# Optimization experiments

Hardware: AMD Instinct MI355X
Metric: run time of the kernel (lower is better)

## Reference

```python
import jax, jax.numpy as jnp
import numpy as np

N = 100000
E = 1600000
IN_F, HID, OUT_F = 256, 128, 64


def setup_inputs() -> dict:
    key = jax.random.key(0)
    k_x, k_e, k_w1, k_w2, k_b1, k_b2 = jax.random.split(key, 6)
    x = jax.random.normal(k_x, (N, IN_F), dtype=jnp.float32)
    edge_index = jax.random.randint(k_e, (2, E), 0, N, dtype=jnp.int32)
    # GCNConv params: lin has no bias in PyG; separate additive bias per layer.
    W1 = jax.random.normal(k_w1, (IN_F, HID), dtype=jnp.float32) / np.sqrt(IN_F)
    b1 = jax.random.normal(k_b1, (HID,), dtype=jnp.float32) * 0.01
    W2 = jax.random.normal(k_w2, (HID, OUT_F), dtype=jnp.float32) / np.sqrt(HID)
    b2 = jax.random.normal(k_b2, (OUT_F,), dtype=jnp.float32) * 0.01
    return {"x": x, "edge_index": edge_index, "W1": W1, "b1": b1, "W2": W2, "b2": b2}


def _gcn_norm(edge_index, num_nodes):
    # add self loops (improved=False -> weight 1.0), symmetric normalization
    loop = jnp.arange(num_nodes, dtype=edge_index.dtype)
    src = jnp.concatenate([edge_index[0], loop])
    dst = jnp.concatenate([edge_index[1], loop])
    w = jnp.ones(src.shape[0], dtype=jnp.float32)
    deg = jax.ops.segment_sum(w, dst, num_segments=num_nodes)
    dinv = jnp.where(deg > 0, jax.lax.rsqrt(deg), 0.0)
    norm = dinv[src] * w * dinv[dst]
    return src, dst, norm


def _gcn_layer(h, W, b, src, dst, norm, num_nodes):
    h = h @ W                               # [N, out]
    msg = h[src] * norm[:, None]            # [E+N, out] gather + scale
    out = jax.ops.segment_sum(msg, dst, num_segments=num_nodes)  # scatter-add
    return out + b


def reference(x, edge_index, W1, b1, W2, b2):
    # dropout is identity in eval mode
    src, dst, norm = _gcn_norm(edge_index, N)
    h = _gcn_layer(x, W1, b1, src, dst, norm, N)
    h = jax.nn.relu(h)
    out = _gcn_layer(h, W2, b2, src, dst, norm, N)
    return out
```

## Files before the change

### kernel.cpp

```cpp
#include <hip/hip_runtime.h>
#include <hip/hip_bf16.h>

#define N_NODES 100000
#define N_EDGES 1600000
#define IN_FEAT 256
#define HID_F   128
#define OUT_FT  64

#define NBUK   256
#define NPB    391
#define BUKCAP 8192
#define EPB    4096
#define G_BIN  ((N_EDGES + EPB - 1) / EPB)
#define G_GEMM ((N_NODES + 63) / 64)
#define G_CAST ((IN_FEAT * HID_F + HID_F * OUT_FT + 255) / 256)
#define G_AGG  ((N_NODES + 7) / 8)

typedef unsigned short u16;
typedef __attribute__((ext_vector_type(8))) unsigned short u16x8;
typedef __attribute__((ext_vector_type(8))) short short8;
typedef __attribute__((ext_vector_type(4))) float f32x4;

static __device__ inline u16 f2bf(float f) {
    __hip_bfloat16 h = __float2bfloat16(f);
    return *reinterpret_cast<u16*>(&h);
}
static __device__ inline float bf2f(u16 u) {
    union { unsigned u; float f; } c;
    c.u = ((unsigned)u) << 16;
    return c.f;
}


__global__ __launch_bounds__(256) void k_bin(const int* __restrict__ srcA,
                                             const int* __restrict__ dstA,
                                             int* __restrict__ gcur, unsigned* __restrict__ pairs,
                                             const float* __restrict__ W1,
                                             const float* __restrict__ W2,
                                             u16* __restrict__ W1t, u16* __restrict__ W2t) {
    if (blockIdx.x >= G_BIN) {
        int idx = (blockIdx.x - G_BIN) * 256 + threadIdx.x;
        if (idx < IN_FEAT * HID_F) {
            int k = idx / HID_F, n = idx % HID_F;
            W1t[n * IN_FEAT + k] = f2bf(W1[idx]);
        } else {
            int e2 = idx - IN_FEAT * HID_F;
            if (e2 < HID_F * OUT_FT) {
                int k = e2 / OUT_FT, n = e2 % OUT_FT;
                W2t[n * HID_F + k] = f2bf(W2[e2]);
            }
        }
        return;
    }
    __shared__ int lh[NBUK];
    int t = threadIdx.x;
    int e0 = blockIdx.x * EPB;
    if (t < NBUK) lh[t] = 0;
    __syncthreads();
#pragma unroll
    for (int i = 0; i < EPB / 256; i++) {
        int e = e0 + i * 256 + t;
        if (e < N_EDGES) atomicAdd(&lh[dstA[e] / NPB], 1);
    }
    __syncthreads();
    if (t < NBUK) {
        int c = lh[t];
        lh[t] = atomicAdd(&gcur[t], c);
    }
    __syncthreads();
#pragma unroll
    for (int i = 0; i < EPB / 256; i++) {
        int e = e0 + i * 256 + t;
        if (e < N_EDGES) {
            int d = dstA[e];
            int b = d / NPB;
            int p = atomicAdd(&lh[b], 1);
            if (p < BUKCAP) {
                unsigned packed = ((unsigned)(d - b * NPB) << 17) | (unsigned)srcA[e];
                pairs[(size_t)b * BUKCAP + p] = packed;
            }
        }
    }
}


__global__ __launch_bounds__(256) void k_fillB(const unsigned* __restrict__ pairs,
                                               const int* __restrict__ gcnt,
                                               int* __restrict__ offsets,
                                               float* __restrict__ dinv,
                                               int* __restrict__ csr) {
    __shared__ int hist[NPB];
    __shared__ int sm[256];
    __shared__ int s_ebase;
    int b = blockIdx.x, t = threadIdx.x;
    int nbase = b * NPB;
    int nn = min(NPB, N_NODES - nbase);

    int gv = gcnt[t];
    sm[t] = gv;
    __syncthreads();
    for (int o = 1; o < 256; o <<= 1) {
        int u = (t >= o) ? sm[t - o] : 0;
        __syncthreads();
        sm[t] += u;
        __syncthreads();
    }
    if (t == b) s_ebase = sm[t] - gv;
    __syncthreads();
    int ebase = s_ebase;
    int cnt = gcnt[b];
    const unsigned* pb = pairs + (size_t)b * BUKCAP;

    for (int i = t; i < NPB; i += 256) hist[i] = 0;
    __syncthreads();
    for (int i = t; i < cnt; i += 256) atomicAdd(&hist[pb[i] >> 17], 1);
    __syncthreads();

    int base2 = t * 2;
    int c0 = (base2 < NPB) ? hist[base2] : 0;
    int c1 = (base2 + 1 < NPB) ? hist[base2 + 1] : 0;
    int s = c0 + c1;
    __syncthreads();
    sm[t] = s;
    __syncthreads();
    for (int o = 1; o < 256; o <<= 1) {
        int u = (t >= o) ? sm[t - o] : 0;
        __syncthreads();
        sm[t] += u;
        __syncthreads();
    }
    int run = ebase + sm[t] - s;
    __syncthreads();
    int cc[2] = {c0, c1};
#pragma unroll
    for (int q = 0; q < 2; q++) {
        int n = base2 + q;
        if (n < nn) {
            int g = nbase + n;
            offsets[g] = run;
            dinv[g] = rsqrtf((float)(cc[q] + 1));
            hist[n] = run;
            run += cc[q];
        }
    }
    __syncthreads();
    for (int i = t; i < cnt; i += 256) {
        unsigned e = pb[i];
        int p = atomicAdd(&hist[e >> 17], 1);
        csr[p] = (int)(e & 0x1FFFFu);
    }
    if (b == NBUK - 1 && t == 0) offsets[N_NODES] = N_EDGES;
}


__global__ __launch_bounds__(256) void k_gemm1(const float* __restrict__ A,
                                               const u16* __restrict__ Bt,
                                               const float* __restrict__ dinv,
                                               u16* __restrict__ C) {
    __shared__ u16 As[2][64][40];
    __shared__ u16 Bs[2][128][40];
    int tid = threadIdx.x;
    int wv = tid >> 6, lane = tid & 63;
    int m16 = lane & 15, quad = lane >> 4;
    int row0 = blockIdx.x * 64;

    int ar = tid >> 2, aq = tid & 3;
    int br = tid >> 1, bh = tid & 1;
    int arow_g = row0 + ar;
    if (arow_g >= N_NODES) arow_g = N_NODES - 1;
    const float* ap = &A[(size_t)arow_g * IN_FEAT + aq * 8];
    const u16*   bp = &Bt[(size_t)br * IN_FEAT + bh * 16];

    f32x4 acc[8];
#pragma unroll
    for (int j = 0; j < 8; j++) acc[j] = (f32x4)(0.f);

    {
        f32x4 a0 = *(const f32x4*)&ap[0];
        f32x4 a1 = *(const f32x4*)&ap[4];
        u16x8 b0 = *(const u16x8*)&bp[0];
        u16x8 b1 = *(const u16x8*)&bp[8];
        u16x8 av;
#pragma unroll
        for (int j = 0; j < 4; j++) { av[j] = f2bf(a0[j]); av[4 + j] = f2bf(a1[j]); }
        *(u16x8*)&As[0][ar][aq * 8] = av;
        *(u16x8*)&Bs[0][br][bh * 16] = b0;
        *(u16x8*)&Bs[0][br][bh * 16 + 8] = b1;
    }

#pragma unroll
    for (int s = 0; s < 8; s++) {
        const int buf = s & 1;
        f32x4 na0, na1; u16x8 nb0, nb1;
        if (s + 1 < 8) {
            int k0 = (s + 1) * 32;
            na0 = *(const f32x4*)&ap[k0];
            na1 = *(const f32x4*)&ap[k0 + 4];
            nb0 = *(const u16x8*)&bp[k0];
            nb1 = *(const u16x8*)&bp[k0 + 8];
        }
        __syncthreads();
        short8 af = *(const short8*)&As[buf][wv * 16 + m16][quad * 8];
#pragma unroll
        for (int ct = 0; ct < 8; ct++) {
            short8 bf = *(const short8*)&Bs[buf][16 * ct + m16][quad * 8];
            acc[ct] = __builtin_amdgcn_mfma_f32_16x16x32_bf16(af, bf, acc[ct], 0, 0, 0);
        }
        if (s + 1 < 8) {
            u16x8 av;
#pragma unroll
            for (int j = 0; j < 4; j++) { av[j] = f2bf(na0[j]); av[4 + j] = f2bf(na1[j]); }
            *(u16x8*)&As[buf ^ 1][ar][aq * 8] = av;
            *(u16x8*)&Bs[buf ^ 1][br][bh * 16] = nb0;
            *(u16x8*)&Bs[buf ^ 1][br][bh * 16 + 8] = nb1;
        }
    }

#pragma unroll
    for (int r4 = 0; r4 < 4; r4++) {
        int grow = row0 + wv * 16 + quad * 4 + r4;
        if (grow < N_NODES) {
            float dv = dinv[grow];
#pragma unroll
            for (int ct = 0; ct < 8; ct++)
                C[(size_t)grow * HID_F + 16 * ct + m16] = f2bf(acc[ct][r4] * dv);
        }
    }
}


__global__ __launch_bounds__(256) void k_gemm2(const u16* __restrict__ A,
                                               const u16* __restrict__ Bt,
                                               const float* __restrict__ dinv,
                                               u16* __restrict__ C) {
    __shared__ u16 As[2][64][40];
    __shared__ u16 Bs[2][64][40];
    int tid = threadIdx.x;
    int wv = tid >> 6, lane = tid & 63;
    int m16 = lane & 15, quad = lane >> 4;
    int row0 = blockIdx.x * 64;

    int ar = tid >> 2, aq = tid & 3;
    int arow_g = row0 + ar;
    if (arow_g >= N_NODES) arow_g = N_NODES - 1;
    const u16* ap = &A[(size_t)arow_g * HID_F + aq * 8];
    const u16* bp = &Bt[(size_t)ar * HID_F + aq * 8];

    f32x4 acc[4];
#pragma unroll
    for (int j = 0; j < 4; j++) acc[j] = (f32x4)(0.f);

    {
        u16x8 a0 = *(const u16x8*)&ap[0];
        u16x8 b0 = *(const u16x8*)&bp[0];
        *(u16x8*)&As[0][ar][aq * 8] = a0;
        *(u16x8*)&Bs[0][ar][aq * 8] = b0;
    }

#pragma unroll
    for (int s = 0; s < 4; s++) {
        const int buf = s & 1;
        u16x8 na, nb;
        if (s + 1 < 4) {
            int k0 = (s + 1) * 32;
            na = *(const u16x8*)&ap[k0];
            nb = *(const u16x8*)&bp[k0];
        }
        __syncthreads();
        short8 af = *(const short8*)&As[buf][wv * 16 + m16][quad * 8];
#pragma unroll
        for (int ct = 0; ct < 4; ct++) {
            short8 bf = *(const short8*)&Bs[buf][16 * ct + m16][quad * 8];
            acc[ct] = __builtin_amdgcn_mfma_f32_16x16x32_bf16(af, bf, acc[ct], 0, 0, 0);
        }
        if (s + 1 < 4) {
            *(u16x8*)&As[buf ^ 1][ar][aq * 8] = na;
            *(u16x8*)&Bs[buf ^ 1][ar][aq * 8] = nb;
        }
    }

#pragma unroll
    for (int r4 = 0; r4 < 4; r4++) {
        int grow = row0 + wv * 16 + quad * 4 + r4;
        if (grow < N_NODES) {
            float dv = dinv[grow];
#pragma unroll
            for (int ct = 0; ct < 4; ct++)
                C[(size_t)grow * OUT_FT + 16 * ct + m16] = f2bf(acc[ct][r4] * dv);
        }
    }
}


__global__ __launch_bounds__(256) void k_agg1(const u16* __restrict__ hs,
                                              const int* __restrict__ offsets,
                                              const int* __restrict__ csr,
                                              const float* __restrict__ dinv,
                                              const float* __restrict__ b,
                                              u16* __restrict__ out) {
    int wave = threadIdx.x >> 6;
    int lane = threadIdx.x & 63;
    int half = lane >> 5;
    int node = blockIdx.x * 8 + wave * 2 + half;
    if (node >= N_NODES) return;
    int gl = lane & 31;
    int g = gl >> 4;
    int fl = gl & 15;
    const int fo = fl * 8;
    int beg = offsets[node], end = offsets[node + 1];

    float accA[8], accB[8];
#pragma unroll
    for (int i = 0; i < 8; i++) { accA[i] = 0.f; accB[i] = 0.f; }

    int j = beg;
    for (; j + 8 <= end; j += 8) {
        int s0 = csr[j + g];
        int s1 = csr[j + 2 + g];
        int s2 = csr[j + 4 + g];
        int s3 = csr[j + 6 + g];
        u16x8 r0 = *(const u16x8*)&hs[(size_t)s0 * HID_F + fo];
        u16x8 r1 = *(const u16x8*)&hs[(size_t)s1 * HID_F + fo];
        u16x8 r2 = *(const u16x8*)&hs[(size_t)s2 * HID_F + fo];
        u16x8 r3 = *(const u16x8*)&hs[(size_t)s3 * HID_F + fo];
#pragma unroll
        for (int i = 0; i < 8; i++) {
            accA[i] += bf2f(r0[i]) + bf2f(r1[i]);
            accB[i] += bf2f(r2[i]) + bf2f(r3[i]);
        }
    }
    if (j + 4 <= end) {
        int s0 = csr[j + g];
        int s1 = csr[j + 2 + g];
        u16x8 r0 = *(const u16x8*)&hs[(size_t)s0 * HID_F + fo];
        u16x8 r1 = *(const u16x8*)&hs[(size_t)s1 * HID_F + fo];
#pragma unroll
        for (int i = 0; i < 8; i++) accA[i] += bf2f(r0[i]) + bf2f(r1[i]);
        j += 4;
    }
    for (; j < end; j += 2) {
        int idx = j + g;
        if (idx < end) {
            int s = csr[idx];
            u16x8 r0 = *(const u16x8*)&hs[(size_t)s * HID_F + fo];
#pragma unroll
            for (int i = 0; i < 8; i++) accB[i] += bf2f(r0[i]);
        }
    }
#pragma unroll
    for (int i = 0; i < 8; i++) {
        float v = accA[i] + accB[i];
        v += __shfl_xor(v, 16, 64);
        accA[i] = v;
    }
    if (g == 0) {
        u16x8 sr = *(const u16x8*)&hs[(size_t)node * HID_F + fo];
        float dv = dinv[node];
        f32x4 b0 = *(const f32x4*)&b[fo];
        f32x4 b1 = *(const f32x4*)&b[fo + 4];
        u16x8 o;
#pragma unroll
        for (int i = 0; i < 4; i++) {
            o[i]     = f2bf(fmaxf(dv * (accA[i]     + bf2f(sr[i]))     + b0[i], 0.f));
            o[4 + i] = f2bf(fmaxf(dv * (accA[4 + i] + bf2f(sr[4 + i])) + b1[i], 0.f));
        }
        *(u16x8*)&out[(size_t)node * HID_F + fo] = o;
    }
}


__global__ __launch_bounds__(256) void k_agg2(const u16* __restrict__ hs,
                                              const int* __restrict__ offsets,
                                              const int* __restrict__ csr,
                                              const float* __restrict__ dinv,
                                              const float* __restrict__ b,
                                              float* __restrict__ out) {
    int wave = threadIdx.x >> 6;
    int lane = threadIdx.x & 63;
    int half = lane >> 5;
    int node = blockIdx.x * 8 + wave * 2 + half;
    if (node >= N_NODES) return;
    int gl = lane & 31;
    int g = gl >> 3;
    int fl = gl & 7;
    const int fo = fl * 8;
    int beg = offsets[node], end = offsets[node + 1];

    float accA[8], accB[8];
#pragma unroll
    for (int i = 0; i < 8; i++) { accA[i] = 0.f; accB[i] = 0.f; }

    int j = beg;
    for (; j + 16 <= end; j += 16) {
        int s0 = csr[j + g];
        int s1 = csr[j + 4 + g];
        int s2 = csr[j + 8 + g];
        int s3 = csr[j + 12 + g];
        u16x8 r0 = *(const u16x8*)&hs[(size_t)s0 * OUT_FT + fo];
        u16x8 r1 = *(const u16x8*)&hs[(size_t)s1 * OUT_FT + fo];
        u16x8 r2 = *(const u16x8*)&hs[(size_t)s2 * OUT_FT + fo];
        u16x8 r3 = *(const u16x8*)&hs[(size_t)s3 * OUT_FT + fo];
#pragma unroll
        for (int i = 0; i < 8; i++) {
            accA[i] += bf2f(r0[i]) + bf2f(r1[i]);
            accB[i] += bf2f(r2[i]) + bf2f(r3[i]);
        }
    }
    if (j + 8 <= end) {
        int s0 = csr[j + g];
        int s1 = csr[j + 4 + g];
        u16x8 r0 = *(const u16x8*)&hs[(size_t)s0 * OUT_FT + fo];
        u16x8 r1 = *(const u16x8*)&hs[(size_t)s1 * OUT_FT + fo];
#pragma unroll
        for (int i = 0; i < 8; i++) accA[i] += bf2f(r0[i]) + bf2f(r1[i]);
        j += 8;
    }
    for (; j < end; j += 4) {
        int idx = j + g;
        if (idx < end) {
            int s = csr[idx];
            u16x8 r0 = *(const u16x8*)&hs[(size_t)s * OUT_FT + fo];
#pragma unroll
            for (int i = 0; i < 8; i++) accB[i] += bf2f(r0[i]);
        }
    }
#pragma unroll
    for (int i = 0; i < 8; i++) {
        float v = accA[i] + accB[i];
        v += __shfl_xor(v, 8, 64);
        v += __shfl_xor(v, 16, 64);
        accA[i] = v;
    }
    if (g == 0) {
        u16x8 sr = *(const u16x8*)&hs[(size_t)node * OUT_FT + fo];
        float dv = dinv[node];
        f32x4 b0 = *(const f32x4*)&b[fo];
        f32x4 b1 = *(const f32x4*)&b[fo + 4];
        f32x4 o0, o1;
#pragma unroll
        for (int i = 0; i < 4; i++) {
            o0[i] = dv * (accA[i]     + bf2f(sr[i]))     + b0[i];
            o1[i] = dv * (accA[4 + i] + bf2f(sr[4 + i])) + b1[i];
        }
        *(f32x4*)&out[(size_t)node * OUT_FT + fo] = o0;
        *(f32x4*)&out[(size_t)node * OUT_FT + fo + 4] = o1;
    }
}


extern "C" void kernel_launch(void* const* d_in, const int* in_sizes, int n_in,
                              void* d_out, int out_size, void* d_ws, size_t ws_size,
                              hipStream_t stream) {
    const float* x  = (const float*)d_in[0];
    const int*   ei = (const int*)d_in[1];
    const float* W1 = (const float*)d_in[2];
    const float* b1 = (const float*)d_in[3];
    const float* W2 = (const float*)d_in[4];
    const float* b2 = (const float*)d_in[5];
    float* out = (float*)d_out;

    char* ws = (char*)d_ws;
    int*   offsets = (int*)(ws + 0);
    float* dinv    = (float*)(ws + 400512);
    int*   csr     = (int*)(ws + 800512);
    u16*   W1t     = (u16*)(ws + 7200512);
    u16*   W2t     = (u16*)(ws + 7266048);
    int*   gcur    = (int*)(ws + 7282432);
    u16*   hs1     = (u16*)(ws + 7284608);
    u16*   a1      = (u16*)(ws + 32884608);
    unsigned* pairs = (unsigned*)(ws + 32884608);
    u16*   hs2     = hs1;

    const int* srcA = ei;
    const int* dstA = ei + N_EDGES;

    hipMemsetAsync(gcur, 0, NBUK * sizeof(int), stream);

    k_bin<<<G_BIN + G_CAST, 256, 0, stream>>>(srcA, dstA, gcur, pairs, W1, W2, W1t, W2t);
    k_fillB<<<NBUK, 256, 0, stream>>>(pairs, gcur, offsets, dinv, csr);

    k_gemm1<<<G_GEMM, 256, 0, stream>>>(x, W1t, dinv, hs1);
    k_agg1<<<G_AGG, 256, 0, stream>>>(hs1, offsets, csr, dinv, b1, a1);
    k_gemm2<<<G_GEMM, 256, 0, stream>>>(a1, W2t, dinv, hs2);
    k_agg2<<<G_AGG, 256, 0, stream>>>(hs2, offsets, csr, dinv, b2, out);
}
```

Measured before the change: 335.5 us.

## Fuse all GCN stages into one cooperative persistent kernel with grid syncs

Turns each stage kernel into a device function and runs all six stages inside one cooperative persistent kernel. Stages are separated by grid-wide syncs, and the original multi-launch path is kept as a fallback if the cooperative launch fails. This removes per-kernel launch gaps and tail drain between stages. The cost is a grid sized by occupancy that loops over virtual blocks, which may lower occupancy because every stage shares the largest shared-memory footprint and register usage. EPB is also halved, giving more binning blocks.

```diff
diff --git a/kernel.cpp b/kernel.cpp
--- a/kernel.cpp
+++ b/kernel.cpp
@@ -1,5 +1,8 @@
 #include <hip/hip_runtime.h>
 #include <hip/hip_bf16.h>
+#include <hip/hip_cooperative_groups.h>
+
+namespace cg = cooperative_groups;
 
 #define N_NODES 100000
 #define N_EDGES 1600000
@@ -10,7 +13,7 @@
 #define NBUK   256
 #define NPB    391
 #define BUKCAP 8192
-#define EPB    4096
+#define EPB    2048
 #define G_BIN  ((N_EDGES + EPB - 1) / EPB)
 #define G_GEMM ((N_NODES + 63) / 64)
 #define G_CAST ((IN_FEAT * HID_F + HID_F * OUT_FT + 255) / 256)
@@ -32,14 +35,13 @@
 }
 
 
-__global__ __launch_bounds__(256) void k_bin(const int* __restrict__ srcA,
-                                             const int* __restrict__ dstA,
-                                             int* __restrict__ gcur, unsigned* __restrict__ pairs,
-                                             const float* __restrict__ W1,
-                                             const float* __restrict__ W2,
-                                             u16* __restrict__ W1t, u16* __restrict__ W2t) {
-    if (blockIdx.x >= G_BIN) {
-        int idx = (blockIdx.x - G_BIN) * 256 + threadIdx.x;
+static __device__ __forceinline__ void dev_bin(int vb, int t, int* lh,
+        const int* __restrict__ srcA, const int* __restrict__ dstA,
+        int* __restrict__ gcur, unsigned* __restrict__ pairs,
+        const float* __restrict__ W1, const float* __restrict__ W2,
+        u16* __restrict__ W1t, u16* __restrict__ W2t) {
+    if (vb >= G_BIN) {
+        int idx = (vb - G_BIN) * 256 + t;
         if (idx < IN_FEAT * HID_F) {
             int k = idx / HID_F, n = idx % HID_F;
             W1t[n * IN_FEAT + k] = f2bf(W1[idx]);
@@ -52,9 +54,8 @@
         }
         return;
     }
-    __shared__ int lh[NBUK];
-    int t = threadIdx.x;
-    int e0 = blockIdx.x * EPB;
+    __syncthreads();
+    int e0 = vb * EPB;
     if (t < NBUK) lh[t] = 0;
     __syncthreads();
 #pragma unroll
@@ -83,16 +84,13 @@
     }
 }
 
-
-__global__ __launch_bounds__(256) void k_fillB(const unsigned* __restrict__ pairs,
-                                               const int* __restrict__ gcnt,
-                                               int* __restrict__ offsets,
-                                               float* __restrict__ dinv,
-                                               int* __restrict__ csr) {
-    __shared__ int hist[NPB];
-    __shared__ int sm[256];
-    __shared__ int s_ebase;
-    int b = blockIdx.x, t = threadIdx.x;
+static __device__ __forceinline__ void dev_fillB(int b, int t, int* shm,
+        const unsigned* __restrict__ pairs, const int* __restrict__ gcnt,
+        int* __restrict__ offsets, float* __restrict__ dinv, int* __restrict__ csr) {
+    int* hist = shm;
+    int* sm   = shm + NPB;
+    int* seb  = shm + NPB + 256;
+    __syncthreads();
     int nbase = b * NPB;
     int nn = min(NPB, N_NODES - nbase);
 
@@ -105,9 +103,9 @@
         sm[t] += u;
         __syncthreads();
     }
-    if (t == b) s_ebase = sm[t] - gv;
-    __syncthreads();
-    int ebase = s_ebase;
+    if (t == b) *seb = sm[t] - gv;
+    __syncthreads();
+    int ebase = *seb;
     int cnt = gcnt[b];
     const unsigned* pb = pairs + (size_t)b * BUKCAP;
 
@@ -152,17 +150,15 @@
     if (b == NBUK - 1 && t == 0) offsets[N_NODES] = N_EDGES;
 }
 
-
-__global__ __launch_bounds__(256) void k_gemm1(const float* __restrict__ A,
-                                               const u16* __restrict__ Bt,
-                                               const float* __restrict__ dinv,
-                                               u16* __restrict__ C) {
-    __shared__ u16 As[2][64][40];
-    __shared__ u16 Bs[2][128][40];
-    int tid = threadIdx.x;
+static __device__ __forceinline__ void dev_gemm1(int vb, int tid, char* smem,
+        const float* __restrict__ A, const u16* __restrict__ Bt,
+        const float* __restrict__ dinv, u16* __restrict__ C) {
+    u16 (*As)[64][40]  = (u16 (*)[64][40])smem;
+    u16 (*Bs)[128][40] = (u16 (*)[128][40])(smem + 10240);
+    __syncthreads();
     int wv = tid >> 6, lane = tid & 63;
     int m16 = lane & 15, quad = lane >> 4;
-    int row0 = blockIdx.x * 64;
+    int row0 = vb * 64;
 
     int ar = tid >> 2, aq = tid & 3;
     int br = tid >> 1, bh = tid & 1;
@@ -228,17 +224,15 @@
     }
 }
 
-
-__global__ __launch_bounds__(256) void k_gemm2(const u16* __restrict__ A,
-                                               const u16* __restrict__ Bt,
-                                               const float* __restrict__ dinv,
-                                               u16* __restrict__ C) {
-    __shared__ u16 As[2][64][40];
-    __shared__ u16 Bs[2][64][40];
-    int tid = threadIdx.x;
+static __device__ __forceinline__ void dev_gemm2(int vb, int tid, char* smem,
+        const u16* __restrict__ A, const u16* __restrict__ Bt,
+        const float* __restrict__ dinv, u16* __restrict__ C) {
+    u16 (*As)[64][40] = (u16 (*)[64][40])smem;
+    u16 (*Bs)[64][40] = (u16 (*)[64][40])(smem + 10240);
+    __syncthreads();
     int wv = tid >> 6, lane = tid & 63;
     int m16 = lane & 15, quad = lane >> 4;
-    int row0 = blockIdx.x * 64;
+    int row0 = vb * 64;
 
     int ar = tid >> 2, aq = tid & 3;
     int arow_g = row0 + ar;
@@ -291,17 +285,14 @@
     }
 }
 
-
-__global__ __launch_bounds__(256) void k_agg1(const u16* __restrict__ hs,
-                                              const int* __restrict__ offsets,
-                                              const int* __restrict__ csr,
-                                              const float* __restrict__ dinv,
-                                              const float* __restrict__ b,
-                                              u16* __restrict__ out) {
-    int wave = threadIdx.x >> 6;
-    int lane = threadIdx.x & 63;
+static __device__ __forceinline__ void dev_agg1(int vb, int tid,
+        const u16* __restrict__ hs, const int* __restrict__ offsets,
+        const int* __restrict__ csr, const float* __restrict__ dinv,
+        const float* __restrict__ b, u16* __restrict__ out) {
+    int wave = tid >> 6;
+    int lane = tid & 63;
     int half = lane >> 5;
-    int node = blockIdx.x * 8 + wave * 2 + half;
+    int node = vb * 8 + wave * 2 + half;
     if (node >= N_NODES) return;
     int gl = lane & 31;
     int g = gl >> 4;
@@ -368,17 +359,14 @@
     }
 }
 
-
-__global__ __launch_bounds__(256) void k_agg2(const u16* __restrict__ hs,
-                                              const int* __restrict__ offsets,
-                                              const int* __restrict__ csr,
-                                              const float* __restrict__ dinv,
-                                              const float* __restrict__ b,
-                                              float* __restrict__ out) {
-    int wave = threadIdx.x >> 6;
-    int lane = threadIdx.x & 63;
+static __device__ __forceinline__ void dev_agg2(int vb, int tid,
+        const u16* __restrict__ hs, const int* __restrict__ offsets,
+        const int* __restrict__ csr, const float* __restrict__ dinv,
+        const float* __restrict__ b, float* __restrict__ out) {
+    int wave = tid >> 6;
+    int lane = tid & 63;
     int half = lane >> 5;
-    int node = blockIdx.x * 8 + wave * 2 + half;
+    int node = vb * 8 + wave * 2 + half;
     if (node >= N_NODES) return;
     int gl = lane & 31;
     int g = gl >> 3;
@@ -448,6 +436,87 @@
 }
 
 
+__global__ __launch_bounds__(256) void k_bin(const int* srcA, const int* dstA,
+        int* gcur, unsigned* pairs, const float* W1, const float* W2,
+        u16* W1t, u16* W2t) {
+    __shared__ int lh[NBUK];
+    dev_bin(blockIdx.x, threadIdx.x, lh, srcA, dstA, gcur, pairs, W1, W2, W1t, W2t);
+}
+
+__global__ __launch_bounds__(256) void k_fillB(const unsigned* pairs, const int* gcnt,
+        int* offsets, float* dinv, int* csr) {
+    __shared__ int shm[NPB + 256 + 1];
+    dev_fillB(blockIdx.x, threadIdx.x, shm, pairs, gcnt, offsets, dinv, csr);
+}
+
+__global__ __launch_bounds__(256) void k_gemm1(const float* A, const u16* Bt,
+        const float* dinv, u16* C) {
+    __shared__ __align__(16) char smem[30720];
+    dev_gemm1(blockIdx.x, threadIdx.x, smem, A, Bt, dinv, C);
+}
+
+__global__ __launch_bounds__(256) void k_gemm2(const u16* A, const u16* Bt,
+        const float* dinv, u16* C) {
+    __shared__ __align__(16) char smem[20480];
+    dev_gemm2(blockIdx.x, threadIdx.x, smem, A, Bt, dinv, C);
+}
+
+__global__ __launch_bounds__(256) void k_agg1(const u16* hs, const int* offsets,
+        const int* csr, const float* dinv, const float* b, u16* out) {
+    dev_agg1(blockIdx.x, threadIdx.x, hs, offsets, csr, dinv, b, out);
+}
+
+__global__ __launch_bounds__(256) void k_agg2(const u16* hs, const int* offsets,
+        const int* csr, const float* dinv, const float* b, float* out) {
+    dev_agg2(blockIdx.x, threadIdx.x, hs, offsets, csr, dinv, b, out);
+}
+
+
+__global__ __launch_bounds__(256) void k_mega(const float* x, const int* ei,
+        const float* W1, const float* b1, const float* W2, const float* b2,
+        float* out, char* ws) {
+    cg::grid_group grid = cg::this_grid();
+    __shared__ __align__(16) char smem[30720];
+    const int bid = blockIdx.x, t = threadIdx.x, G = gridDim.x;
+
+    int*      offsets = (int*)(ws + 0);
+    float*    dinv    = (float*)(ws + 400512);
+    int*      csr     = (int*)(ws + 800512);
+    u16*      W1t     = (u16*)(ws + 7200512);
+    u16*      W2t     = (u16*)(ws + 7266048);
+    int*      gcur    = (int*)(ws + 7282432);
+    u16*      hs1     = (u16*)(ws + 7284608);
+    u16*      a1      = (u16*)(ws + 32884608);
+    unsigned* pairs   = (unsigned*)(ws + 32884608);
+    u16*      hs2     = hs1;
+    const int* srcA = ei;
+    const int* dstA = ei + N_EDGES;
+
+    for (int vb = bid; vb < G_BIN + G_CAST; vb += G)
+        dev_bin(vb, t, (int*)smem, srcA, dstA, gcur, pairs, W1, W2, W1t, W2t);
+    __threadfence(); grid.sync();
+
+    for (int vb = bid; vb < NBUK; vb += G)
+        dev_fillB(vb, t, (int*)smem, pairs, gcur, offsets, dinv, csr);
+    __threadfence(); grid.sync();
+
+    for (int vb = bid; vb < G_GEMM; vb += G)
+        dev_gemm1(vb, t, smem, x, W1t, dinv, hs1);
+    __threadfence(); grid.sync();
+
+    for (int vb = bid; vb < G_AGG; vb += G)
+        dev_agg1(vb, t, hs1, offsets, csr, dinv, b1, a1);
+    __threadfence(); grid.sync();
+
+    for (int vb = bid; vb < G_GEMM; vb += G)
+        dev_gemm2(vb, t, smem, a1, W2t, dinv, hs2);
+    __threadfence(); grid.sync();
+
+    for (int vb = bid; vb < G_AGG; vb += G)
+        dev_agg2(vb, t, hs2, offsets, csr, dinv, b2, out);
+}
+
+
 extern "C" void kernel_launch(void* const* d_in, const int* in_sizes, int n_in,
                               void* d_out, int out_size, void* d_ws, size_t ws_size,
                               hipStream_t stream) {
@@ -460,27 +529,40 @@
     float* out = (float*)d_out;
 
     char* ws = (char*)d_ws;
-    int*   offsets = (int*)(ws + 0);
-    float* dinv    = (float*)(ws + 400512);
-    int*   csr     = (int*)(ws + 800512);
-    u16*   W1t     = (u16*)(ws + 7200512);
-    u16*   W2t     = (u16*)(ws + 7266048);
-    int*   gcur    = (int*)(ws + 7282432);
-    u16*   hs1     = (u16*)(ws + 7284608);
-    u16*   a1      = (u16*)(ws + 32884608);
-    unsigned* pairs = (unsigned*)(ws + 32884608);
-    u16*   hs2     = hs1;
+    int*      offsets = (int*)(ws + 0);
+    float*    dinv    = (float*)(ws + 400512);
+    int*      csr     = (int*)(ws + 800512);
+    u16*      W1t     = (u16*)(ws + 7200512);
+    u16*      W2t     = (u16*)(ws + 7266048);
+    int*      gcur    = (int*)(ws + 7282432);
+    u16*      hs1     = (u16*)(ws + 7284608);
+    u16*      a1      = (u16*)(ws + 32884608);
+    unsigned* pairs   = (unsigned*)(ws + 32884608);
+    u16*      hs2     = hs1;
 
     const int* srcA = ei;
     const int* dstA = ei + N_EDGES;
 
     hipMemsetAsync(gcur, 0, NBUK * sizeof(int), stream);
 
-    k_bin<<<G_BIN + G_CAST, 256, 0, stream>>>(srcA, dstA, gcur, pairs, W1, W2, W1t, W2t);
-    k_fillB<<<NBUK, 256, 0, stream>>>(pairs, gcur, offsets, dinv, csr);
-
-    k_gemm1<<<G_GEMM, 256, 0, stream>>>(x, W1t, dinv, hs1);
-    k_agg1<<<G_AGG, 256, 0, stream>>>(hs1, offsets, csr, dinv, b1, a1);
-    k_gemm2<<<G_GEMM, 256, 0, stream>>>(a1, W2t, dinv, hs2);
-    k_agg2<<<G_AGG, 256, 0, stream>>>(hs2, offsets, csr, dinv, b2, out);
-}
+    int nb = 0;
+    hipError_t qerr = hipOccupancyMaxActiveBlocksPerMultiprocessor(&nb, k_mega, 256, 0);
+    int ncu = 0;
+    if (hipDeviceGetAttribute(&ncu, hipDeviceAttributeMultiprocessorCount, 0) != hipSuccess || ncu <= 0)
+        ncu = 256;
+    hipError_t lerr = hipErrorInvalidValue;
+    if (qerr == hipSuccess && nb > 0) {
+        int grid = nb * ncu;
+        void* kargs[] = { (void*)&x, (void*)&ei, (void*)&W1, (void*)&b1, (void*)&W2,
+                          (void*)&b2, (void*)&out, (void*)&ws };
+        lerr = hipLaunchCooperativeKernel(k_mega, dim3(grid), dim3(256), kargs, 0, stream);
+    }
+    if (lerr != hipSuccess) {
+        k_bin<<<G_BIN + G_CAST, 256, 0, stream>>>(srcA, dstA, gcur, pairs, W1, W2, W1t, W2t);
+        k_fillB<<<NBUK, 256, 0, stream>>>(pairs, gcur, offsets, dinv, csr);
+        k_gemm1<<<G_GEMM, 256, 0, stream>>>(x, W1t, dinv, hs1);
+        k_agg1<<<G_AGG, 256, 0, stream>>>(hs1, offsets, csr, dinv, b1, a1);
+        k_gemm2<<<G_GEMM, 256, 0, stream>>>(a1, W2t, dinv, hs2);
+        k_agg2<<<G_AGG, 256, 0, stream>>>(hs2, offsets, csr, dinv, b2, out);
+    }
+}
```

New measurement: 1.039 ms. 3.1x slower.
